# Kernel tuning notes

Hardware: AMD Instinct MI355X
Metric: run time of the kernel (lower is better)

## Reference

```python
import jax, jax.numpy as jnp
import numpy as np

NMS_THRE = 0.4
NEG = -1e30  # sentinel for sort key of suppressed boxes


def _iou_adjacency(boxes, nms_thre):
    # boxes: [N,4] in cxcywh -> xyxy, then dense IoU >= thre adjacency (no self loops)
    cx, cy, w, h = boxes[:, 0], boxes[:, 1], boxes[:, 2], boxes[:, 3]
    x1 = cx - w / 2
    y1 = cy - h / 2
    x2 = x1 + w
    y2 = y1 + h
    b = jnp.stack([x1, y1, x2, y2], axis=-1)  # [N,4]
    area = (x2 - x1) * (y2 - y1)
    lt = jnp.maximum(b[:, None, :2], b[None, :, :2])  # [N,N,2]
    rb = jnp.minimum(b[:, None, 2:], b[None, :, 2:])
    wh = jnp.clip(rb - lt, 0.0)
    inter = wh[..., 0] * wh[..., 1]
    iou = inter / (area[:, None] + area[None, :] - inter)
    n = boxes.shape[0]
    return (iou >= nms_thre) & (~jnp.eye(n, dtype=bool))


def _greedy_suppress(valid0, adj, scores):
    # Sequential greedy NMS over candidates in descending score order.
    # valid shrinks monotonically, and valid <= valid0 always, so clearing
    # neighbors via adj row exactly matches the torch loop (which only clears
    # neighbors that were initially valid -- already-false entries are no-ops).
    order = jnp.argsort(-scores)

    def body(k, valid):
        idx = order[k]
        return jnp.where(valid[idx], valid & (~adj[idx]), valid)

    return jax.lax.fori_loop(0, scores.shape[0], body, valid0)


def _per_class(pro_c, con_c, conf_c, adj):
    # scatter_max over adjacency: max of con over neighbors (0 if no neighbors,
    # matching torch_scatter's zero-init)
    adj_con = jnp.max(jnp.where(adj, con_c[None, :], 0.0), axis=1)
    valid0 = (pro_c >= conf_c) & (pro_c >= adj_con) & (pro_c >= con_c)
    return _greedy_suppress(valid0, adj, pro_c)


def _per_image(pro, con, boxes, scale, conf_thres):
    # pro/con: [N,C]; boxes: [N,4] cxcywh; scale: scalar; conf_thres: [C]
    adj = _iou_adjacency(boxes, NMS_THRE)
    survive = jax.vmap(_per_class, in_axes=(1, 1, 0, None))(pro, con, conf_thres, adj)  # [C,N]
    b = boxes * scale
    cx, cy, w, h = b[:, 0], b[:, 1], b[:, 2], b[:, 3]
    xyxy = jnp.stack([cx - 0.5 * w, cy - 0.5 * h, cx + 0.5 * w, cy + 0.5 * h], axis=-1)  # [N,4]
    scores = pro.T  # [C,N]
    C = scores.shape[0]
    bws = jnp.concatenate(
        [jnp.broadcast_to(xyxy[None], (C,) + xyxy.shape), scores[..., None]], axis=-1
    )  # [C,N,5]
    bws = bws * survive[..., None].astype(bws.dtype)  # zero out suppressed rows
    key = jnp.where(survive, scores, NEG)
    perm = jnp.argsort(-key, axis=1)  # per-class descending score order
    bws = jnp.take_along_axis(bws, perm[..., None], axis=1)
    mask = jnp.take_along_axis(survive, perm, axis=1)
    return bws, mask


def setup_inputs() -> dict:
    key = jax.random.key(0)
    k1, k2, k3, k4 = jax.random.split(key, 4)
    B, N, C = 4, 3600, 16
    return {
        "pro_max": jax.random.uniform(k1, (B, N, C), dtype=jnp.float32),
        "con_max": jax.random.uniform(k2, (B, N, C), dtype=jnp.float32),
        "pred_boxes": jax.random.uniform(k3, (B, N, 4), dtype=jnp.float32),
        "image_scales": jax.random.uniform(k4, (B,), dtype=jnp.float32),
        "conf_thres": jnp.zeros((C,), dtype=jnp.float32),
    }


def reference(pro_max, con_max, pred_boxes, image_scales, conf_thres):
    # Returns (boxes_with_scores [B,C,N,5] sorted per class by score desc,
    #          survive_mask [B,C,N] aligned with the sorted rows).
    return jax.vmap(_per_image, in_axes=(0, 0, 0, 0, None))(
        pro_max, con_max, pred_boxes, image_scales, conf_thres
    )
```

## Files before the change

kernel.cpp:

```cpp
#include <hip/hip_runtime.h>
#include <cstdint>

typedef unsigned long long u64;
typedef unsigned int u32;

#define B_ 4
#define N_ 3600
#define C_ 16
#define NW_ 57
#define NPAD_ 3648
#define RPW_ 4
#define RPB_ 16
#define TPI_ 1596
#define CH_ 64
#define NT_ 512
#define NWV_ 8
#define RPWG_ 8

__global__ __launch_bounds__(256) void k_adj(const float* __restrict__ boxes,
                                             u64* __restrict__ adj) {
#pragma clang fp contract(off)
    const int tid  = threadIdx.x;
    const int lane = tid & 63;
    const int wv   = tid >> 6;
    const int g    = blockIdx.x;
    const int b    = g / (N_ / RPB_);
    const int rg   = g % (N_ / RPB_);
    const int r0   = rg * RPB_ + wv * RPW_;
    const int w0   = rg >> 2;
    const size_t bN = (size_t)b * N_;

    float4 bi[RPW_];
    float  ai[RPW_];
#pragma unroll
    for (int r = 0; r < RPW_; ++r) {
        const float4 bx = reinterpret_cast<const float4*>(boxes)[bN + r0 + r];
        const float x1 = bx.x - bx.z * 0.5f;
        const float y1 = bx.y - bx.w * 0.5f;
        const float x2 = x1 + bx.z;
        const float y2 = y1 + bx.w;
        bi[r] = make_float4(x1, y1, x2, y2);
        ai[r] = (x2 - x1) * (y2 - y1);
    }
    const double MID = (double)0.4f - 0x1p-26;

    u64 row[RPW_];
#pragma unroll
    for (int r = 0; r < RPW_; ++r) row[r] = 0ull;

    for (int tw = w0; tw < NW_; ++tw) {
        const int j  = tw * 64 + lane;
        const int jc = min(j, N_ - 1);
        const float4 bx = reinterpret_cast<const float4*>(boxes)[bN + jc];
        float x1 = bx.x - bx.z * 0.5f;
        float y1 = bx.y - bx.w * 0.5f;
        float x2 = x1 + bx.z;
        float y2 = y1 + bx.w;
        if (j >= N_) { x1 = 0.f; y1 = 0.f; x2 = 0.f; y2 = 0.f; }
        const float ajr = (x2 - x1) * (y2 - y1);
#pragma unroll
        for (int r = 0; r < RPW_; ++r) {
            const float ltx = fmaxf(bi[r].x, x1);
            const float lty = fmaxf(bi[r].y, y1);
            const float rbx = fminf(bi[r].z, x2);
            const float rby = fminf(bi[r].w, y2);
            const float whx = fmaxf(rbx - ltx, 0.0f);
            const float why = fmaxf(rby - lty, 0.0f);
            const float inter = whx * why;
            const float denom = (ai[r] + ajr) - inter;
            const int pred = ((double)inter > MID * (double)denom);
            const u64 m = __ballot(pred);
            if (lane == tw) row[r] = m;
        }
    }

#pragma unroll
    for (int r = 0; r < RPW_; ++r)
        if (lane == w0) row[r] &= ~(1ull << ((r0 + r) & 63));

#pragma unroll
    for (int r = 0; r < RPW_; ++r)
        if (lane >= w0 && lane < NW_)
            adj[(bN + r0 + r) * (size_t)NW_ + lane] = row[r];
}

__global__ __launch_bounds__(256) void k_tr(u64* __restrict__ adj) {
    const int lane = threadIdx.x & 63;
    const int wv   = threadIdx.x >> 6;
    const int p    = blockIdx.x * 4 + wv;
    const int b    = p / TPI_;
    const int p2   = p % TPI_;
    int wi = (int)((1.0f + sqrtf((float)(8 * p2 + 1))) * 0.5f);
    while (wi * (wi - 1) / 2 > p2) --wi;
    while ((wi + 1) * wi / 2 <= p2) ++wi;
    const int wj = p2 - wi * (wi - 1) / 2;
    const size_t bN = (size_t)b * N_;

    u64 x = adj[(bN + wj * 64 + lane) * (size_t)NW_ + wi];

    const u64 M[6] = {0x00000000FFFFFFFFull, 0x0000FFFF0000FFFFull,
                      0x00FF00FF00FF00FFull, 0x0F0F0F0F0F0F0F0Full,
                      0x3333333333333333ull, 0x5555555555555555ull};
#pragma unroll
    for (int si = 0; si < 6; ++si) {
        const int s = 32 >> si;
        const u64 m = M[si];
        const u64 t = __shfl_xor(x, s);
        x = ((lane & s) == 0) ? ((x & m) | ((t & m) << s))
                              : ((x & ~m) | ((t & ~m) >> s));
    }

    const int rowi = wi * 64 + lane;
    if (rowi < N_)
        adj[(bN + rowi) * (size_t)NW_ + wj] = x;
}

__global__ __launch_bounds__(256) void k_acon(const u64* __restrict__ adj,
                                              const float* __restrict__ con,
                                              float* __restrict__ thr) {
    const int tid  = threadIdx.x;
    const int lane = tid & 63;
    const int wv   = tid >> 6;
    const int g    = blockIdx.x;
    const int b    = g / (N_ / 4);
    const int i    = (g % (N_ / 4)) * 4 + wv;
    const size_t bN = (size_t)b * N_;

    u64 w = (lane < NW_) ? adj[(bN + i) * (size_t)NW_ + lane] : 0ull;

    float cm[C_];
#pragma unroll
    for (int k = 0; k < C_; ++k) cm[k] = 0.0f;

    while (w) {
        const int bit = __builtin_ctzll(w); w &= w - 1;
        const int j   = lane * 64 + bit;
        const float4* cp = reinterpret_cast<const float4*>(con + (bN + j) * C_);
        const float4 c0 = cp[0], c1 = cp[1], c2 = cp[2], c3 = cp[3];
        cm[0]  = fmaxf(cm[0],  c0.x); cm[1]  = fmaxf(cm[1],  c0.y);
        cm[2]  = fmaxf(cm[2],  c0.z); cm[3]  = fmaxf(cm[3],  c0.w);
        cm[4]  = fmaxf(cm[4],  c1.x); cm[5]  = fmaxf(cm[5],  c1.y);
        cm[6]  = fmaxf(cm[6],  c1.z); cm[7]  = fmaxf(cm[7],  c1.w);
        cm[8]  = fmaxf(cm[8],  c2.x); cm[9]  = fmaxf(cm[9],  c2.y);
        cm[10] = fmaxf(cm[10], c2.z); cm[11] = fmaxf(cm[11], c2.w);
        cm[12] = fmaxf(cm[12], c3.x); cm[13] = fmaxf(cm[13], c3.y);
        cm[14] = fmaxf(cm[14], c3.z); cm[15] = fmaxf(cm[15], c3.w);
    }

#pragma unroll
    for (int off = 1; off < 64; off <<= 1) {
#pragma unroll
        for (int k = 0; k < C_; ++k) cm[k] = fmaxf(cm[k], __shfl_xor(cm[k], off));
    }
    if (lane == 0) {
        const float4* cp = reinterpret_cast<const float4*>(con + (bN + i) * C_);
        const float4 c0 = cp[0], c1 = cp[1], c2 = cp[2], c3 = cp[3];
        float4* o = reinterpret_cast<float4*>(thr + (bN + i) * C_);
        o[0] = make_float4(fmaxf(cm[0],  c0.x), fmaxf(cm[1],  c0.y),
                           fmaxf(cm[2],  c0.z), fmaxf(cm[3],  c0.w));
        o[1] = make_float4(fmaxf(cm[4],  c1.x), fmaxf(cm[5],  c1.y),
                           fmaxf(cm[6],  c1.z), fmaxf(cm[7],  c1.w));
        o[2] = make_float4(fmaxf(cm[8],  c2.x), fmaxf(cm[9],  c2.y),
                           fmaxf(cm[10], c2.z), fmaxf(cm[11], c2.w));
        o[3] = make_float4(fmaxf(cm[12], c3.x), fmaxf(cm[13], c3.y),
                           fmaxf(cm[14], c3.z), fmaxf(cm[15], c3.w));
    }
}

union OvT {
    u64 keys[NPAD_];
    u64 srows[2][CH_][NW_];
};

__global__ __launch_bounds__(NT_) void k_nms(const float* __restrict__ pro,
                                             const float* __restrict__ thr,
                                             const float* __restrict__ conf,
                                             const u64* __restrict__ adj,
                                             const float* __restrict__ boxes,
                                             const float* __restrict__ scales,
                                             float* __restrict__ out) {
#pragma clang fp contract(off)
    __shared__ OvT ov;
    __shared__ u32 sidx[NPAD_];
    __shared__ u64 sintra[CH_];
    __shared__ u64 vmask[NW_];
    __shared__ u64 s_accept;
    __shared__ u32 slist[NPAD_];
    __shared__ u32 s_T;
    __shared__ u32 s_S;
    const int tid  = threadIdx.x;
    const int lane = tid & 63;
    const int wv   = tid >> 6;
    const int bc   = blockIdx.x;
    const int b    = bc / C_, c = bc % C_;
    const size_t bN = (size_t)b * N_;
    const float cf = conf[c];

    if (tid == 0) s_T = 0;
    __syncthreads();

    for (int t = wv; t < NW_; t += NWV_) {
        const int i = t * 64 + lane;
        int pred = 0;
        u32 pk = 0;
        if (i < N_) {
            const size_t off = (bN + i) * C_ + c;
            const float p = pro[off];
            pred = (p >= cf) && (p >= thr[off]);
            const u32 pb = __float_as_uint(p);
            pk = pb ^ ((pb >> 31) ? 0xFFFFFFFFu : 0x80000000u);
        }
        const u64 bm = __ballot(pred);
        if (lane == 0) vmask[t] = bm;
        u32 base = 0;
        if (lane == 0 && bm) base = atomicAdd(&s_T, (u32)__popcll(bm));
        base = (u32)__shfl((int)base, 0);
        if (pred) ov.keys[base + (u32)__popcll(bm & ((1ull << lane) - 1ull))] =
            (((u64)(~pk)) << 32) | (u32)i;
    }
    __syncthreads();

    const int T = (int)s_T;
    for (int k = 0; k * NT_ < T; ++k) {
        const int x  = tid + k * NT_;
        const u64 kx = (x < T) ? ov.keys[x] : ~0ull;
        u32 rank = 0;
        for (int y = 0; y < T; ++y) rank += (ov.keys[y] < kx);
        if (x < T) sidx[rank] = (u32)(kx & 0xFFFFFFFFull);
    }
    __syncthreads();

#pragma unroll
    for (int rr = 0; rr < RPWG_; ++rr) {
        const int r = wv * RPWG_ + rr;
        const u32 idx = (r < T) ? sidx[r] : 0u;
        if (lane < NW_) ov.srows[0][r][lane] = adj[(bN + idx) * (size_t)NW_ + lane];
    }
    __syncthreads();

    u32 S = 0;
    const int NCH = (T + CH_ - 1) / CH_;
    for (int ch = 0; ch < NCH; ++ch) {
        const int cur = ch & 1, nxt = cur ^ 1;
        const int c0 = ch * CH_;
        const int cn = min(CH_, T - c0);
        const int havenext = (ch + 1 < NCH);

        u64 pre[RPWG_];
#pragma unroll
        for (int rr = 0; rr < RPWG_; ++rr) {
            const int r = wv * RPWG_ + rr;
            const int q = c0 + CH_ + r;
            const u32 idxn = (havenext && q < T) ? sidx[q] : 0u;
            pre[rr] = (havenext && lane < NW_)
                        ? adj[(bN + idxn) * (size_t)NW_ + lane] : 0ull;
        }
#pragma unroll
        for (int rr = 0; rr < RPWG_; ++rr) {
            const int r = wv * RPWG_ + rr;
            const u32 idxr = (c0 + r < T) ? sidx[c0 + r] : 0u;
            const u64 rj = ov.srows[cur][lane][idxr >> 6];
            const u64 ib = __ballot((lane < cn) && ((rj >> (idxr & 63)) & 1ull));
            if (lane == 0) sintra[r] = ib;
        }
        __syncthreads();

        if (wv == 0) {
            const u32 idxme = (c0 + lane < T) ? sidx[c0 + lane] : 0u;
            const u64 vm = vmask[idxme >> 6];
            u64 cv = __ballot((lane < cn) && ((vm >> (idxme & 63)) & 1ull));
            const u64 iv = sintra[lane];
            const u32 ivLo = (u32)iv, ivHi = (u32)(iv >> 32);
            u64 accept = 0ull;
            while (cv) {
                const int r = __builtin_ctzll(cv);
                accept |= 1ull << r;
                const u64 ir =
                    ((u64)(u32)__builtin_amdgcn_readlane((int)ivHi, r) << 32)
                  |  (u64)(u32)__builtin_amdgcn_readlane((int)ivLo, r);
                cv &= ~(ir | (1ull << r));
            }
            if (lane == 0) s_accept = accept;
            const u32 bitl = (u32)((accept >> lane) & 1ull);
            if (bitl) {
                const u32 pos = S + (u32)__popcll(accept & ((1ull << lane) - 1ull));
                slist[pos] = idxme;
            }
            S += (u32)__popcll(accept);
        }
        __syncthreads();

        const u64 ac = s_accept;
        u64 acc = 0ull;
#pragma unroll
        for (int rr = 0; rr < RPWG_; ++rr) {
            const int r = wv * RPWG_ + rr;
            if ((ac >> r) & 1ull)
                acc |= ov.srows[cur][r][min(lane, NW_ - 1)];
        }
        if (lane < NW_ && acc)
            atomicAnd(&vmask[lane], ~acc);
        if (havenext) {
#pragma unroll
            for (int rr = 0; rr < RPWG_; ++rr) {
                const int r = wv * RPWG_ + rr;
                if (lane < NW_) ov.srows[nxt][r][lane] = pre[rr];
            }
        }
        __syncthreads();
    }
    if (wv == 0 && lane == 0) s_S = S;
    __syncthreads();

    const int Sf = (int)s_S;
    const float s = scales[b];
    for (int r = tid; r < N_; r += NT_) {
        float o0 = 0.f, o1 = 0.f, o2 = 0.f, o3 = 0.f, o4 = 0.f, mk = 0.f;
        if (r < Sf) {
            const int idx = (int)slist[r];
            const float4 bx = reinterpret_cast<const float4*>(boxes)[bN + idx];
            const float scx = bx.x * s, scy = bx.y * s;
            const float sw  = bx.z * s, sh  = bx.w * s;
            o0 = scx - 0.5f * sw;
            o1 = scy - 0.5f * sh;
            o2 = scx + 0.5f * sw;
            o3 = scy + 0.5f * sh;
            o4 = pro[(bN + idx) * C_ + c];
            mk = 1.0f;
        }
        float* o = out + ((size_t)bc * N_ + r) * 5;
        o[0] = o0; o[1] = o1; o[2] = o2; o[3] = o3; o[4] = o4;
        out[(size_t)B_ * C_ * N_ * 5 + (size_t)bc * N_ + r] = mk;
    }
}

extern "C" void kernel_launch(void* const* d_in, const int* in_sizes, int n_in,
                              void* d_out, int out_size, void* d_ws, size_t ws_size,
                              hipStream_t stream) {
    const float* pro    = (const float*)d_in[0];
    const float* con    = (const float*)d_in[1];
    const float* boxes  = (const float*)d_in[2];
    const float* scales = (const float*)d_in[3];
    const float* conf   = (const float*)d_in[4];

    char* ws = (char*)d_ws;
    u64* adj = (u64*)ws;
    size_t off = (size_t)B_ * N_ * NW_ * sizeof(u64);
    float* thr = (float*)(ws + off);

    k_adj <<<B_ * N_ / RPB_,    256, 0, stream>>>(boxes, adj);
    k_tr  <<<B_ * TPI_ / 4,     256, 0, stream>>>(adj);
    k_acon<<<B_ * N_ / 4,       256, 0, stream>>>(adj, con, thr);
    k_nms <<<B_ * C_,           NT_, 0, stream>>>(pro, thr, conf, adj, boxes,
                                                  scales, (float*)d_out);
}
```

Baseline: 175.1 us.

## Stage boxes in LDS for IoU and move candidate filtering into acon kernel

k_adj now converts the column boxes once per block into shared memory in two halves instead of having every wave reload and convert them from global memory. k_acon applies the per-class threshold test itself and appends sort keys to per-class candidate lists through global atomics, so the thr buffer and the per-class pro scan in k_nms go away. k_nms reads the compacted candidates, builds vmask from them, and carries scores through shared memory so it no longer re-reads pro at output time. This adds global atomic contention and a counter reset inside k_tr, plus extra shared-memory footprint in k_nms.

```diff
diff --git a/kernel.cpp b/kernel.cpp
--- a/kernel.cpp
+++ b/kernel.cpp
@@ -12,14 +12,17 @@
 #define RPW_ 4
 #define RPB_ 16
 #define TPI_ 1596
+#define HW0_ 1856
+#define HW1_ 1792
 #define CH_ 64
 #define NT_ 512
 #define NWV_ 8
 #define RPWG_ 8
 
-__global__ __launch_bounds__(256) void k_adj(const float* __restrict__ boxes,
-                                             u64* __restrict__ adj) {
+__global__ __launch_bounds__(256, 4) void k_adj(const float* __restrict__ boxes,
+                                                u64* __restrict__ adj) {
 #pragma clang fp contract(off)
+    __shared__ float4 sbox[HW0_];
     const int tid  = threadIdx.x;
     const int lane = tid & 63;
     const int wv   = tid >> 6;
@@ -48,30 +51,50 @@
 #pragma unroll
     for (int r = 0; r < RPW_; ++r) row[r] = 0ull;
 
-    for (int tw = w0; tw < NW_; ++tw) {
-        const int j  = tw * 64 + lane;
-        const int jc = min(j, N_ - 1);
-        const float4 bx = reinterpret_cast<const float4*>(boxes)[bN + jc];
-        float x1 = bx.x - bx.z * 0.5f;
-        float y1 = bx.y - bx.w * 0.5f;
-        float x2 = x1 + bx.z;
-        float y2 = y1 + bx.w;
-        if (j >= N_) { x1 = 0.f; y1 = 0.f; x2 = 0.f; y2 = 0.f; }
-        const float ajr = (x2 - x1) * (y2 - y1);
-#pragma unroll
-        for (int r = 0; r < RPW_; ++r) {
-            const float ltx = fmaxf(bi[r].x, x1);
-            const float lty = fmaxf(bi[r].y, y1);
-            const float rbx = fminf(bi[r].z, x2);
-            const float rby = fminf(bi[r].w, y2);
-            const float whx = fmaxf(rbx - ltx, 0.0f);
-            const float why = fmaxf(rby - lty, 0.0f);
-            const float inter = whx * why;
-            const float denom = (ai[r] + ajr) - inter;
-            const int pred = ((double)inter > MID * (double)denom);
-            const u64 m = __ballot(pred);
-            if (lane == tw) row[r] = m;
-        }
+    int jbase = 0;
+    for (int h = 0; h < 2; ++h) {
+        const int cnt  = h ? HW1_ : HW0_;
+        const int wlo  = jbase >> 6;
+        const int wcnt = cnt >> 6;
+        if (w0 < wlo + wcnt) {
+            const int tw0 = max(w0 - wlo, 0);
+            const int jj0 = tw0 << 6;
+            __syncthreads();
+            for (int jj = jj0 + tid; jj < cnt; jj += 256) {
+                const int j = jbase + jj;
+                float x1 = 0.f, y1 = 0.f, x2 = 0.f, y2 = 0.f;
+                if (j < N_) {
+                    const float4 bx = reinterpret_cast<const float4*>(boxes)[bN + j];
+                    x1 = bx.x - bx.z * 0.5f;
+                    y1 = bx.y - bx.w * 0.5f;
+                    x2 = x1 + bx.z;
+                    y2 = y1 + bx.w;
+                }
+                sbox[jj] = make_float4(x1, y1, x2, y2);
+            }
+            __syncthreads();
+
+            for (int tw = tw0; tw < wcnt; ++tw) {
+                const int tglob = wlo + tw;
+                const float4 bj = sbox[tw * 64 + lane];
+                const float ajr = (bj.z - bj.x) * (bj.w - bj.y);
+#pragma unroll
+                for (int r = 0; r < RPW_; ++r) {
+                    const float ltx = fmaxf(bi[r].x, bj.x);
+                    const float lty = fmaxf(bi[r].y, bj.y);
+                    const float rbx = fminf(bi[r].z, bj.z);
+                    const float rby = fminf(bi[r].w, bj.w);
+                    const float whx = fmaxf(rbx - ltx, 0.0f);
+                    const float why = fmaxf(rby - lty, 0.0f);
+                    const float inter = whx * why;
+                    const float denom = (ai[r] + ajr) - inter;
+                    const int pred = ((double)inter > MID * (double)denom);
+                    const u64 m = __ballot(pred);
+                    if (lane == tglob) row[r] = m;
+                }
+            }
+        }
+        jbase += cnt;
     }
 
 #pragma unroll
@@ -84,7 +107,11 @@
             adj[(bN + r0 + r) * (size_t)NW_ + lane] = row[r];
 }
 
-__global__ __launch_bounds__(256) void k_tr(u64* __restrict__ adj) {
+__global__ __launch_bounds__(256) void k_tr(u64* __restrict__ adj,
+                                            u32* __restrict__ cnt) {
+    if (blockIdx.x == 0) {
+        for (int x = threadIdx.x; x < B_ * C_ * 16; x += 256) cnt[x] = 0;
+    }
     const int lane = threadIdx.x & 63;
     const int wv   = threadIdx.x >> 6;
     const int p    = blockIdx.x * 4 + wv;
@@ -117,7 +144,10 @@
 
 __global__ __launch_bounds__(256) void k_acon(const u64* __restrict__ adj,
                                               const float* __restrict__ con,
-                                              float* __restrict__ thr) {
+                                              const float* __restrict__ pro,
+                                              const float* __restrict__ conf,
+                                              u64* __restrict__ cand,
+                                              u32* __restrict__ cnt) {
     const int tid  = threadIdx.x;
     const int lane = tid & 63;
     const int wv   = tid >> 6;
@@ -155,15 +185,33 @@
     if (lane == 0) {
         const float4* cp = reinterpret_cast<const float4*>(con + (bN + i) * C_);
         const float4 c0 = cp[0], c1 = cp[1], c2 = cp[2], c3 = cp[3];
-        float4* o = reinterpret_cast<float4*>(thr + (bN + i) * C_);
-        o[0] = make_float4(fmaxf(cm[0],  c0.x), fmaxf(cm[1],  c0.y),
-                           fmaxf(cm[2],  c0.z), fmaxf(cm[3],  c0.w));
-        o[1] = make_float4(fmaxf(cm[4],  c1.x), fmaxf(cm[5],  c1.y),
-                           fmaxf(cm[6],  c1.z), fmaxf(cm[7],  c1.w));
-        o[2] = make_float4(fmaxf(cm[8],  c2.x), fmaxf(cm[9],  c2.y),
-                           fmaxf(cm[10], c2.z), fmaxf(cm[11], c2.w));
-        o[3] = make_float4(fmaxf(cm[12], c3.x), fmaxf(cm[13], c3.y),
-                           fmaxf(cm[14], c3.z), fmaxf(cm[15], c3.w));
+        const float4* pp = reinterpret_cast<const float4*>(pro + (bN + i) * C_);
+        const float4 p0 = pp[0], p1 = pp[1], p2 = pp[2], p3 = pp[3];
+        const float4* fp = reinterpret_cast<const float4*>(conf);
+        const float4 f0 = fp[0], f1 = fp[1], f2 = fp[2], f3 = fp[3];
+        const float th[C_] = {
+            fmaxf(cm[0],  c0.x), fmaxf(cm[1],  c0.y),
+            fmaxf(cm[2],  c0.z), fmaxf(cm[3],  c0.w),
+            fmaxf(cm[4],  c1.x), fmaxf(cm[5],  c1.y),
+            fmaxf(cm[6],  c1.z), fmaxf(cm[7],  c1.w),
+            fmaxf(cm[8],  c2.x), fmaxf(cm[9],  c2.y),
+            fmaxf(cm[10], c2.z), fmaxf(cm[11], c2.w),
+            fmaxf(cm[12], c3.x), fmaxf(cm[13], c3.y),
+            fmaxf(cm[14], c3.z), fmaxf(cm[15], c3.w)};
+        const float pr[C_] = {p0.x, p0.y, p0.z, p0.w, p1.x, p1.y, p1.z, p1.w,
+                              p2.x, p2.y, p2.z, p2.w, p3.x, p3.y, p3.z, p3.w};
+        const float cf[C_] = {f0.x, f0.y, f0.z, f0.w, f1.x, f1.y, f1.z, f1.w,
+                              f2.x, f2.y, f2.z, f2.w, f3.x, f3.y, f3.z, f3.w};
+#pragma unroll
+        for (int k = 0; k < C_; ++k) {
+            if (pr[k] >= cf[k] && pr[k] >= th[k]) {
+                const u32 pb = __float_as_uint(pr[k]);
+                const u32 pk = pb ^ ((pb >> 31) ? 0xFFFFFFFFu : 0x80000000u);
+                const u32 pos = atomicAdd(&cnt[(b * C_ + k) * 16], 1u);
+                cand[(size_t)(b * C_ + k) * N_ + pos] =
+                    (((u64)(~pk)) << 32) | (u32)i;
+            }
+        }
     }
 }
 
@@ -172,9 +220,8 @@
     u64 srows[2][CH_][NW_];
 };
 
-__global__ __launch_bounds__(NT_) void k_nms(const float* __restrict__ pro,
-                                             const float* __restrict__ thr,
-                                             const float* __restrict__ conf,
+__global__ __launch_bounds__(NT_) void k_nms(const u64* __restrict__ cand,
+                                             const u32* __restrict__ cnt,
                                              const u64* __restrict__ adj,
                                              const float* __restrict__ boxes,
                                              const float* __restrict__ scales,
@@ -182,51 +229,39 @@
 #pragma clang fp contract(off)
     __shared__ OvT ov;
     __shared__ u32 sidx[NPAD_];
+    __shared__ float sscore[NPAD_];
     __shared__ u64 sintra[CH_];
     __shared__ u64 vmask[NW_];
     __shared__ u64 s_accept;
     __shared__ u32 slist[NPAD_];
-    __shared__ u32 s_T;
+    __shared__ float slistf[NPAD_];
     __shared__ u32 s_S;
     const int tid  = threadIdx.x;
     const int lane = tid & 63;
     const int wv   = tid >> 6;
     const int bc   = blockIdx.x;
-    const int b    = bc / C_, c = bc % C_;
+    const int b    = bc / C_;
     const size_t bN = (size_t)b * N_;
-    const float cf = conf[c];
-
-    if (tid == 0) s_T = 0;
+
+    const int T = (int)cnt[bc * 16];
+    for (int x = tid; x < T; x += NT_)
+        ov.keys[x] = cand[(size_t)bc * N_ + x];
+    if (tid < NW_) vmask[tid] = 0ull;
     __syncthreads();
 
-    for (int t = wv; t < NW_; t += NWV_) {
-        const int i = t * 64 + lane;
-        int pred = 0;
-        u32 pk = 0;
-        if (i < N_) {
-            const size_t off = (bN + i) * C_ + c;
-            const float p = pro[off];
-            pred = (p >= cf) && (p >= thr[off]);
-            const u32 pb = __float_as_uint(p);
-            pk = pb ^ ((pb >> 31) ? 0xFFFFFFFFu : 0x80000000u);
-        }
-        const u64 bm = __ballot(pred);
-        if (lane == 0) vmask[t] = bm;
-        u32 base = 0;
-        if (lane == 0 && bm) base = atomicAdd(&s_T, (u32)__popcll(bm));
-        base = (u32)__shfl((int)base, 0);
-        if (pred) ov.keys[base + (u32)__popcll(bm & ((1ull << lane) - 1ull))] =
-            (((u64)(~pk)) << 32) | (u32)i;
-    }
-    __syncthreads();
-
-    const int T = (int)s_T;
     for (int k = 0; k * NT_ < T; ++k) {
         const int x  = tid + k * NT_;
         const u64 kx = (x < T) ? ov.keys[x] : ~0ull;
         u32 rank = 0;
         for (int y = 0; y < T; ++y) rank += (ov.keys[y] < kx);
-        if (x < T) sidx[rank] = (u32)(kx & 0xFFFFFFFFull);
+        if (x < T) {
+            const u32 i = (u32)(kx & 0xFFFFFFFFull);
+            sidx[rank] = i;
+            const u32 pk = ~((u32)(kx >> 32));
+            const u32 pb = (pk & 0x80000000u) ? (pk ^ 0x80000000u) : ~pk;
+            sscore[rank] = __uint_as_float(pb);
+            atomicOr(&vmask[i >> 6], 1ull << (i & 63));
+        }
     }
     __syncthreads();
 
@@ -284,7 +319,8 @@
             const u32 bitl = (u32)((accept >> lane) & 1ull);
             if (bitl) {
                 const u32 pos = S + (u32)__popcll(accept & ((1ull << lane) - 1ull));
-                slist[pos] = idxme;
+                slist[pos]  = idxme;
+                slistf[pos] = sscore[c0 + lane];
             }
             S += (u32)__popcll(accept);
         }
@@ -325,7 +361,7 @@
             o1 = scy - 0.5f * sh;
             o2 = scx + 0.5f * sw;
             o3 = scy + 0.5f * sh;
-            o4 = pro[(bN + idx) * C_ + c];
+            o4 = slistf[r];
             mk = 1.0f;
         }
         float* o = out + ((size_t)bc * N_ + r) * 5;
@@ -346,11 +382,13 @@
     char* ws = (char*)d_ws;
     u64* adj = (u64*)ws;
     size_t off = (size_t)B_ * N_ * NW_ * sizeof(u64);
-    float* thr = (float*)(ws + off);
-
-    k_adj <<<B_ * N_ / RPB_,    256, 0, stream>>>(boxes, adj);
-    k_tr  <<<B_ * TPI_ / 4,     256, 0, stream>>>(adj);
-    k_acon<<<B_ * N_ / 4,       256, 0, stream>>>(adj, con, thr);
-    k_nms <<<B_ * C_,           NT_, 0, stream>>>(pro, thr, conf, adj, boxes,
-                                                  scales, (float*)d_out);
-}
+    u64* cand = (u64*)(ws + off);
+    off += (size_t)B_ * C_ * N_ * sizeof(u64);
+    u32* cnt = (u32*)(ws + off);
+
+    k_adj <<<B_ * N_ / RPB_, 256, 0, stream>>>(boxes, adj);
+    k_tr  <<<B_ * TPI_ / 4,  256, 0, stream>>>(adj, cnt);
+    k_acon<<<B_ * N_ / 4,    256, 0, stream>>>(adj, con, pro, conf, cand, cnt);
+    k_nms <<<B_ * C_,        NT_, 0, stream>>>(cand, cnt, adj, boxes,
+                                               scales, (float*)d_out);
+}
```

After: 170.2 us. -2.8%, faster.
